# Kernel optimization log

Measured on AMD Instinct MI355X. Metric: run time of the kernel, lower is better.

Reference implementation:

```python
import jax, jax.numpy as jnp
import numpy as np

DIM = 512; H = 8; TEMP_LEN = 16; TARGET_LEN = 22
NT = TEMP_LEN ** 2          # 256 temp tokens
NS = TARGET_LEN ** 2        # 484 target tokens
N = NT + NS                 # 740
HD = DIM // H
SCALE = HD ** -0.5
EPS = 1e-5
B = 16


def _bias_index(L):
    coords = np.stack(np.meshgrid(np.arange(L), np.arange(L), indexing='ij')).reshape(2, -1)
    rel = (coords[:, :, None] - coords[:, None, :]).transpose(1, 2, 0)  # [L^2, L^2, 2]
    rel[..., 0] += L - 1
    rel[..., 1] += L - 1
    rel[..., 0] *= 2 * L - 1
    return jnp.asarray(rel.sum(-1))  # [L^2, L^2] indices into (2L-1)^2 table

TEMP_IDX = _bias_index(TEMP_LEN)
TARGET_IDX = _bias_index(TARGET_LEN)


def setup_inputs() -> dict:
    key = jax.random.key(0)
    ctr = iter(range(100))
    def nrm(shape, s=1.0):
        return jax.random.normal(jax.random.fold_in(key, next(ctr)), shape, jnp.float32) * s
    def uni(shape):
        return jax.random.uniform(jax.random.fold_in(key, next(ctr)), shape, jnp.float32, 0.5, 1.5)
    d = {'x': nrm((B, N, DIM))}
    for nm in ('q', 'k', 'v'):
        d[f'conv_{nm}_w'] = nrm((DIM, 1, 3, 3), 0.2)   # depthwise 3x3, groups=DIM
        d[f'bn_{nm}_g'] = 1.0 + nrm((DIM,), 0.1)
        d[f'bn_{nm}_b'] = nrm((DIM,), 0.1)
        d[f'bn_{nm}_m'] = nrm((DIM,), 0.1)
        d[f'bn_{nm}_v'] = uni((DIM,))
    for nm in ('q', 'k', 'v', 'p'):
        d[f'w{nm}'] = nrm((DIM, DIM), DIM ** -0.5)
        d[f'b{nm}'] = nrm((DIM,), 0.01)
    d['rpb_target'] = nrm(((2 * TARGET_LEN - 1) ** 2, H), 0.0002)
    d['rpb_temp'] = nrm(((2 * TEMP_LEN - 1) ** 2, 1), 0.0002)
    d['tt_bias'] = nrm((H, 1, NT), 0.0002)       # temp_target_bias_table
    d['tg_tm_bias'] = nrm((H, NS, 1), 0.0002)    # target_temp_bias_table
    return d


def _dwconv_bn(z, w, g, b, m, v):
    # z: [B, C, Hh, Ww]; depthwise conv + BatchNorm2d (inference stats)
    y = jax.lax.conv_general_dilated(z, w, (1, 1), ((1, 1), (1, 1)),
                                     dimension_numbers=('NCHW', 'OIHW', 'NCHW'),
                                     feature_group_count=DIM)
    inv = (g * jax.lax.rsqrt(v + EPS))[None, :, None, None]
    return (y - m[None, :, None, None]) * inv + b[None, :, None, None]


def reference(x, conv_q_w, bn_q_g, bn_q_b, bn_q_m, bn_q_v,
              conv_k_w, bn_k_g, bn_k_b, bn_k_m, bn_k_v,
              conv_v_w, bn_v_g, bn_v_b, bn_v_m, bn_v_v,
              wq, bq, wk, bk, wv, bv, wp, bp,
              rpb_target, rpb_temp, tt_bias, tg_tm_bias):
    Bb = x.shape[0]
    to_img = lambda t, L: t.transpose(0, 2, 1).reshape(Bb, DIM, L, L)
    to_seq = lambda t: t.reshape(Bb, DIM, -1).transpose(0, 2, 1)
    ti = to_img(x[:, :NT], TEMP_LEN)
    tg = to_img(x[:, NT:], TARGET_LEN)

    def conv_branch(w, g, b, m, v):
        return jnp.concatenate([to_seq(_dwconv_bn(ti, w, g, b, m, v)),
                                to_seq(_dwconv_bn(tg, w, g, b, m, v))], axis=1)

    q = conv_branch(conv_q_w, bn_q_g, bn_q_b, bn_q_m, bn_q_v) @ wq + bq
    k = conv_branch(conv_k_w, bn_k_g, bn_k_b, bn_k_m, bn_k_v) @ wk + bk
    v = conv_branch(conv_v_w, bn_v_g, bn_v_b, bn_v_m, bn_v_v) @ wv + bv

    heads = lambda t: t.reshape(Bb, -1, H, HD).transpose(0, 2, 1, 3)
    qtm, ktm, vtm = heads(q[:, :NT]), heads(k[:, :NT]), heads(v[:, :NT])
    qta, kh, vh = heads(q[:, NT:]), heads(k), heads(v)

    # gathered relative-position bias tables
    target_bias = rpb_target[TARGET_IDX.reshape(-1)].reshape(NS, NS, H).transpose(2, 0, 1)  # [H,NS,NS]
    temp_bias = rpb_temp[TEMP_IDX.reshape(-1)].reshape(NT, NT, 1).transpose(2, 0, 1)        # [1,NT,NT]
    padding = tt_bias + tg_tm_bias                                                          # [H,NS,NT]
    rel = jnp.concatenate([padding, target_bias], axis=2)                                   # [H,NS,N]

    # target -> all attention
    attn = jax.nn.softmax(jnp.einsum('bhqd,bhkd->bhqk', qta, kh) * SCALE + rel, axis=-1)
    out_t = jnp.einsum('bhqk,bhkd->bhqd', attn, vh).transpose(0, 2, 1, 3).reshape(Bb, NS, DIM)

    # temp -> temp attention (bias broadcast over heads)
    attn2 = jax.nn.softmax(jnp.einsum('bhqd,bhkd->bhqk', qtm, ktm) * SCALE + temp_bias, axis=-1)
    out_m = jnp.einsum('bhqk,bhkd->bhqd', attn2, vtm).transpose(0, 2, 1, 3).reshape(Bb, NT, DIM)

    return jnp.concatenate([out_m, out_t], axis=1) @ wp + bp
```

## Files before the change

kernel.cpp:

```cpp
#include <hip/hip_runtime.h>
#include <hip/hip_bf16.h>

typedef unsigned short u16;
typedef unsigned int u32;
typedef __attribute__((ext_vector_type(8))) short short8;
typedef __attribute__((ext_vector_type(4))) float f32x4;

#define NTOK 740
#define NTMP 256
#define NTGT 484
#define DM   512
#define MH   8
#define MROWS 11840
#define KPAD 768
#define LOG2E 1.4426950408889634f

__device__ __forceinline__ float b2f(u16 u) {
    union { unsigned int i; float f; } x; x.i = ((unsigned int)u) << 16; return x.f;
}
__device__ __forceinline__ u16 f2b(float f) {
    union { float f; unsigned int i; } x; x.f = f;
    unsigned int r = x.i + 0x7FFFu + ((x.i >> 16) & 1u);
    return (u16)(r >> 16);
}
__device__ __forceinline__ u32 pk2(float a, float b) {
    union { __hip_bfloat162 h; u32 u; } p;
    p.h = __float22bfloat162_rn(float2{a, b});
    return p.u;
}
__device__ __forceinline__ float fexp2(float x) {
    return __builtin_amdgcn_exp2f(x);
}
struct alignas(8) us4 { u16 x, y, z, w; };

__device__ __forceinline__ void gload16(const void* g, void* l) {
    __builtin_amdgcn_global_load_lds(
        (const __attribute__((address_space(1))) void*)g,
        (__attribute__((address_space(3))) void*)l, 16, 0, 0);
}

__global__ __launch_bounds__(256) void transpose4(const float* __restrict__ w0,
                                                  const float* __restrict__ w1,
                                                  const float* __restrict__ w2,
                                                  const float* __restrict__ w3,
                                                  u16* __restrict__ wTbase) {
    __shared__ float t[32][33];
    const int z = blockIdx.z;
    const float* W = z == 0 ? w0 : z == 1 ? w1 : z == 2 ? w2 : w3;
    u16* WT = wTbase + (size_t)z * 262144;
    int bx = blockIdx.x, by = blockIdx.y;
    int tx = threadIdx.x;
    for (int i = threadIdx.y; i < 32; i += 8)
        t[i][tx] = W[(size_t)(by * 32 + i) * 512 + bx * 32 + tx];
    __syncthreads();
    for (int i = threadIdx.y; i < 32; i += 8)
        WT[(size_t)(bx * 32 + i) * 512 + by * 32 + tx] = f2b(t[tx][i]);
}

__global__ __launch_bounds__(512) void prep_conv3(
    const float* __restrict__ cw0, const float* __restrict__ g0, const float* __restrict__ bb0,
    const float* __restrict__ m0, const float* __restrict__ v0,
    const float* __restrict__ cw1, const float* __restrict__ g1, const float* __restrict__ bb1,
    const float* __restrict__ m1, const float* __restrict__ v1,
    const float* __restrict__ cw2, const float* __restrict__ g2, const float* __restrict__ bb2,
    const float* __restrict__ m2, const float* __restrict__ v2,
    float* __restrict__ cwfb, float* __restrict__ shb) {
    const int tap = blockIdx.x, br = blockIdx.y, c = threadIdx.x;
    const float* cw = br == 0 ? cw0 : br == 1 ? cw1 : cw2;
    const float* g  = br == 0 ? g0  : br == 1 ? g1  : g2;
    const float* bb = br == 0 ? bb0 : br == 1 ? bb1 : bb2;
    const float* m  = br == 0 ? m0  : br == 1 ? m1  : m2;
    const float* v  = br == 0 ? v0  : br == 1 ? v1  : v2;
    const float inv = g[c] * rsqrtf(v[c] + 1e-5f);
    cwfb[(br * 9 + tap) * DM + c] = cw[c * 9 + tap] * inv;
    if (tap == 0) shb[br * DM + c] = bb[c] - m[c] * inv;
}

__global__ __launch_bounds__(256) void conv_bn3(
    const float* __restrict__ x,
    const float* __restrict__ cwfb, const float* __restrict__ shb,
    u16* __restrict__ o0, u16* __restrict__ o1, u16* __restrict__ o2) {
    const int bn = blockIdx.x * 2 + (threadIdx.x >> 7);
    const int c = (threadIdx.x & 127) * 4;
    const int b = bn / NTOK, n = bn % NTOK;
    const bool tmp = n < NTMP;
    const int L = tmp ? 16 : 22, base = tmp ? 0 : NTMP, p = n - base;
    const int ph = p / L, pw = p % L;
    float4 xv[9];
#pragma unroll
    for (int tap = 0; tap < 9; ++tap) {
        const int dh = tap / 3 - 1, dw = tap % 3 - 1;
        const int h2 = ph + dh, w2 = pw + dw;
        const bool ok = (h2 >= 0 && h2 < L && w2 >= 0 && w2 < L);
        xv[tap] = ok ? *(const float4*)(x + (size_t)(b * NTOK + base + h2 * L + w2) * DM + c)
                     : float4{0.f, 0.f, 0.f, 0.f};
    }
    const size_t o = (size_t)bn * DM + c;
    u16* out[3] = {o0, o1, o2};
#pragma unroll
    for (int br = 0; br < 3; ++br) {
        float4 acc = *(const float4*)(shb + br * DM + c);
#pragma unroll
        for (int tap = 0; tap < 9; ++tap) {
            const float4 wv = *(const float4*)(cwfb + (br * 9 + tap) * DM + c);
            acc.x = fmaf(wv.x, xv[tap].x, acc.x);
            acc.y = fmaf(wv.y, xv[tap].y, acc.y);
            acc.z = fmaf(wv.z, xv[tap].z, acc.z);
            acc.w = fmaf(wv.w, xv[tap].w, acc.w);
        }
        us4 r;
        r.x = f2b(acc.x); r.y = f2b(acc.y); r.z = f2b(acc.z); r.w = f2b(acc.w);
        *(us4*)(out[br] + o) = r;
    }
}

#define GEMM_BODY(A, BT)                                                             \
    const int tid = threadIdx.x;                                                     \
    const int gm0 = blockIdx.x * 64;                                                 \
    const int gn0 = blockIdx.y * 128;                                                \
    const int lane = tid & 63, w = tid >> 6;                                         \
    const int lr = lane & 15, lg = lane >> 4;                                        \
    const int wm = (w >> 1) * 32, wn = (w & 1) * 64;                                 \
    const int srow4 = lane >> 2;                                                     \
    const int sc = (lane & 3) ^ (srow4 & 3);                                         \
    const u16* asrc  = A  + (size_t)(gm0 + w * 16 + srow4) * 512 + sc * 8;           \
    const u16* bsrc0 = BT + (size_t)(gn0 + w * 32 + srow4) * 512 + sc * 8;           \
    const u16* bsrc1 = BT + (size_t)(gn0 + w * 32 + 16 + srow4) * 512 + sc * 8;      \
    f32x4 acc[2][4] = {};                                                            \
    gload16(asrc, &As[0][w * 512]);                                                  \
    gload16(bsrc0, &Bs[0][w * 1024]);                                                \
    gload16(bsrc1, &Bs[0][w * 1024 + 512]);                                          \
    for (int kt = 0; kt < 16; ++kt) {                                                \
        const int cur = kt & 1;                                                      \
        if (kt < 15) {                                                               \
            gload16(asrc + (kt + 1) * 32, &As[cur ^ 1][w * 512]);                    \
            gload16(bsrc0 + (kt + 1) * 32, &Bs[cur ^ 1][w * 1024]);                  \
            gload16(bsrc1 + (kt + 1) * 32, &Bs[cur ^ 1][w * 1024 + 512]);            \
            asm volatile("s_waitcnt vmcnt(3)" ::: "memory");                         \
        } else {                                                                     \
            asm volatile("s_waitcnt vmcnt(0)" ::: "memory");                         \
        }                                                                            \
        __syncthreads();                                                             \
        short8 af[2], bfr[4];                                                        \
        _Pragma("unroll")                                                            \
        for (int i = 0; i < 2; ++i)                                                  \
            af[i] = *(const short8*)&As[cur][(wm + i * 16 + lr) * 32 + (lg ^ (lr & 3)) * 8]; \
        _Pragma("unroll")                                                            \
        for (int j = 0; j < 4; ++j)                                                  \
            bfr[j] = *(const short8*)&Bs[cur][(wn + j * 16 + lr) * 32 + (lg ^ (lr & 3)) * 8]; \
        _Pragma("unroll")                                                            \
        for (int i = 0; i < 2; ++i)                                                  \
            _Pragma("unroll")                                                        \
            for (int j = 0; j < 4; ++j)                                              \
                acc[i][j] = __builtin_amdgcn_mfma_f32_16x16x32_bf16(af[i], bfr[j], acc[i][j], 0, 0, 0); \
        __syncthreads();                                                             \
    }

__global__ __launch_bounds__(256) void gemm_qkv(
    const u16* __restrict__ Aq, const u16* __restrict__ Ak, const u16* __restrict__ Av,
    const u16* __restrict__ wTb, const float* __restrict__ bq,
    const float* __restrict__ bk, const float* __restrict__ bv,
    u16* __restrict__ qout, u16* __restrict__ kout, u16* __restrict__ vbT, int zbase) {
    __shared__ u16 As[2][64 * 32];
    __shared__ u16 Bs[2][128 * 32];
    const int z = blockIdx.z + zbase;
    const u16* A = z == 0 ? Aq : z == 1 ? Ak : Av;
    const u16* BT = wTb + (size_t)z * 262144;
    const float* bias = z == 0 ? bq : z == 1 ? bk : bv;
    GEMM_BODY(A, BT)
    u16* lin = z == 0 ? qout : kout;
#pragma unroll
    for (int i = 0; i < 2; ++i)
#pragma unroll
        for (int j = 0; j < 4; ++j) {
            const int gc = gn0 + wn + j * 16 + lr;
            const float bvl = bias[gc];
#pragma unroll
            for (int r = 0; r < 4; ++r) {
                const int gr = gm0 + wm + i * 16 + lg * 4 + r;
                const float val = acc[i][j][r] + bvl;
                if (z == 2) {
                    const int b2 = gr / NTOK, k = gr - b2 * NTOK;
                    const int hh = gc >> 6, d = gc & 63;
                    vbT[((size_t)(b2 * MH + hh) * 64 + d) * KPAD + k] = f2b(val);
                } else {
                    lin[(size_t)gr * 512 + gc] = f2b(val);
                }
            }
        }
}

__global__ __launch_bounds__(256) void gemm_out(const u16* __restrict__ Ain,
                                                const u16* __restrict__ BTin,
                                                const float* __restrict__ bias,
                                                float* __restrict__ C) {
    __shared__ u16 As[2][64 * 32];
    __shared__ u16 Bs[2][128 * 32];
    GEMM_BODY(Ain, BTin)
#pragma unroll
    for (int i = 0; i < 2; ++i)
#pragma unroll
        for (int j = 0; j < 4; ++j) {
            const int gc = gn0 + wn + j * 16 + lr;
            const float bvl = bias[gc];
#pragma unroll
            for (int r = 0; r < 4; ++r) {
                const int gr = gm0 + wm + i * 16 + lg * 4 + r;
                C[(size_t)gr * 512 + gc] = acc[i][j][r] + bvl;
            }
        }
}

__global__ __launch_bounds__(256) void build_bias_t(const float* __restrict__ rpb_t,
                                                    const float* __restrict__ tt,
                                                    const float* __restrict__ tg,
                                                    u16* __restrict__ btab) {
    const int q = blockIdx.x, h = blockIdx.y;
    const int qh = q / 22, qw = q % 22;
    const float tgv = tg[h * NTGT + q];
    for (int k = threadIdx.x; k < KPAD; k += 256) {
        float val;
        if (k < NTMP) val = (tt[h * NTMP + k] + tgv) * LOG2E;
        else if (k < NTOK) {
            const int kj = k - NTMP, kh = kj / 22, kw = kj % 22;
            val = rpb_t[((qh - kh + 21) * 43 + (qw - kw + 21)) * MH + h] * LOG2E;
        } else val = -1e30f;
        btab[((size_t)(h * NTGT + q)) * KPAD + k] = f2b(val);
    }
}
__global__ __launch_bounds__(256) void build_bias_m(const float* __restrict__ rpb_m,
                                                    u16* __restrict__ mtab) {
    const int q = blockIdx.x, k = threadIdx.x;
    const int qh = q >> 4, qw = q & 15, kh = k >> 4, kw = k & 15;
    mtab[q * 256 + k] = f2b(rpb_m[(qh - kh + 15) * 31 + (qw - kw + 15)] * LOG2E);
}

__global__ __launch_bounds__(256) void attn_all(const u16* __restrict__ qb,
                                                const u16* __restrict__ kb,
                                                const u16* __restrict__ vbT,
                                                const u16* __restrict__ btab,
                                                const u16* __restrict__ mtab,
                                                u16* __restrict__ attb) {
    __shared__ u16 Ks[2][32][64];
    __shared__ u16 VTs[2][64][32];
    __shared__ u16 Pb[4][16][32];

    const int bx = blockIdx.x, h = blockIdx.y, b = blockIdx.z;
    const bool tgt = bx < 8;
    const int q0 = (tgt ? bx : bx - 8) * 64;
    const int NKr = tgt ? NTOK : NTMP;
    const int NCH = tgt ? 24 : 8;
    const int QTOT = tgt ? NTGT : NTMP;
    const int QOFF = tgt ? NTMP : 0;
    const int tid = threadIdx.x;
    const int w = tid >> 6, lane = tid & 63;
    const int lq = lane & 15, lg = lane >> 4;
    const int fq = (lq & 3) ^ ((lq >> 2) & 3);
    const size_t brow = (size_t)b * NTOK;
    const float SCL = 0.125f * LOG2E;

    int qmine = q0 + w * 16 + lq;
    if (qmine > QTOT - 1) qmine = QTOT - 1;
    const u16* trow = tgt ? (btab + ((size_t)(h * NTGT + qmine)) * KPAD)
                          : (mtab + qmine * 256);

    short8 qf[2];
#pragma unroll
    for (int dc = 0; dc < 2; ++dc)
        qf[dc] = *(const short8*)(qb + (brow + QOFF + qmine) * DM + h * 64 + dc * 32 + lg * 8);

    const int krow = tid >> 3, ksc = tid & 7;
    const int vrow = tid >> 2, vsc = tid & 3;
    const int fv = (vrow & 3) ^ ((vrow >> 2) & 3);
    const u16* kptr = kb + brow * DM + h * 64 + ksc * 8;
    const u16* vptr = vbT + (size_t)(b * MH + h) * 64 * KPAD + (size_t)vrow * KPAD + vsc * 8;

    float mrun = -1e30f, lrun = 0.f;
    f32x4 oT[4] = {};

    {
        int4 kv = (krow < NKr) ? *(const int4*)(kptr + (size_t)krow * DM) : int4{0, 0, 0, 0};
        *(int4*)&Ks[0][krow][(ksc ^ (krow & 7)) * 8] = kv;
        int4 vv = *(const int4*)(vptr);
        *(int4*)&VTs[0][vrow][(vsc ^ fv) * 8] = vv;
    }
    us4 bc0 = *(const us4*)(trow + lg * 4);
    us4 bc1 = *(const us4*)(trow + 16 + lg * 4);
    __syncthreads();

    for (int kc = 0; kc < NCH; ++kc) {
        const int cur = kc & 1, nxt = cur ^ 1;
        const bool more = (kc + 1 < NCH);
        int4 nk = {0, 0, 0, 0}, nv = {0, 0, 0, 0};
        us4 bn0 = {0, 0, 0, 0}, bn1 = {0, 0, 0, 0};
        if (more) {
            const int key = (kc + 1) * 32 + krow;
            if (key < NKr) nk = *(const int4*)(kptr + (size_t)key * DM);
            nv = *(const int4*)(vptr + (kc + 1) * 32);
            bn0 = *(const us4*)(trow + (kc + 1) * 32 + lg * 4);
            bn1 = *(const us4*)(trow + (kc + 1) * 32 + 16 + lg * 4);
        }

        f32x4 s0 = {}, s1 = {};
        __builtin_amdgcn_s_setprio(1);
#pragma unroll
        for (int dc = 0; dc < 2; ++dc) {
            short8 a0 = *(const short8*)&Ks[cur][lq][((dc * 4 + lg) ^ (lq & 7)) * 8];
            short8 a1 = *(const short8*)&Ks[cur][16 + lq][((dc * 4 + lg) ^ (lq & 7)) * 8];
            s0 = __builtin_amdgcn_mfma_f32_16x16x32_bf16(a0, qf[dc], s0, 0, 0, 0);
            s1 = __builtin_amdgcn_mfma_f32_16x16x32_bf16(a1, qf[dc], s1, 0, 0, 0);
        }
        __builtin_amdgcn_s_setprio(0);
        float sv[8];
        sv[0] = fmaf(s0[0], SCL, b2f(bc0.x)); sv[1] = fmaf(s0[1], SCL, b2f(bc0.y));
        sv[2] = fmaf(s0[2], SCL, b2f(bc0.z)); sv[3] = fmaf(s0[3], SCL, b2f(bc0.w));
        sv[4] = fmaf(s1[0], SCL, b2f(bc1.x)); sv[5] = fmaf(s1[1], SCL, b2f(bc1.y));
        sv[6] = fmaf(s1[2], SCL, b2f(bc1.z)); sv[7] = fmaf(s1[3], SCL, b2f(bc1.w));

        float cm = sv[0];
#pragma unroll
        for (int i = 1; i < 8; ++i) cm = fmaxf(cm, sv[i]);
        cm = fmaxf(cm, __shfl_xor(cm, 16));
        cm = fmaxf(cm, __shfl_xor(cm, 32));
        if (!__all(cm <= mrun)) {
            const float mnew = fmaxf(mrun, cm);
            const float alpha = fexp2(mrun - mnew);
#pragma unroll
            for (int t = 0; t < 4; ++t)
#pragma unroll
                for (int r = 0; r < 4; ++r) oT[t][r] *= alpha;
            lrun *= alpha;
            mrun = mnew;
        }
        float pv[8]; float psum = 0.f;
#pragma unroll
        for (int i = 0; i < 8; ++i) { pv[i] = fexp2(sv[i] - mrun); psum += pv[i]; }

        const int c0 = (((lg >> 1) ^ fq) & 3) * 8 + (lg & 1) * 4;
        const int c1 = (((2 + (lg >> 1)) ^ fq) & 3) * 8 + (lg & 1) * 4;
        *(uint2*)&Pb[w][lq][c0] = uint2{pk2(pv[0], pv[1]), pk2(pv[2], pv[3])};
        *(uint2*)&Pb[w][lq][c1] = uint2{pk2(pv[4], pv[5]), pk2(pv[6], pv[7])};

        psum += __shfl_xor(psum, 16);
        psum += __shfl_xor(psum, 32);
        lrun += psum;

        asm volatile("s_waitcnt lgkmcnt(0)" ::: "memory");

        short8 pf = *(const short8*)&Pb[w][lq][((lg ^ fq) & 3) * 8];
        __builtin_amdgcn_s_setprio(1);
#pragma unroll
        for (int t = 0; t < 4; ++t) {
            short8 vf = *(const short8*)&VTs[cur][t * 16 + lq][((lg ^ fq) & 3) * 8];
            oT[t] = __builtin_amdgcn_mfma_f32_16x16x32_bf16(vf, pf, oT[t], 0, 0, 0);
        }
        __builtin_amdgcn_s_setprio(0);

        if (more) {
            *(int4*)&Ks[nxt][krow][(ksc ^ (krow & 7)) * 8] = nk;
            *(int4*)&VTs[nxt][vrow][(vsc ^ fv) * 8] = nv;
            bc0 = bn0; bc1 = bn1;
        }
        __syncthreads();
    }

    const float linv = 1.f / lrun;
    const int qrow = q0 + w * 16 + lq;
    if (qrow < QTOT) {
        u16* op = attb + (brow + QOFF + qrow) * DM + h * 64;
#pragma unroll
        for (int t = 0; t < 4; ++t)
            *(uint2*)(op + t * 16 + lg * 4) =
                uint2{pk2(oT[t][0] * linv, oT[t][1] * linv),
                      pk2(oT[t][2] * linv, oT[t][3] * linv)};
    }
}

extern "C" void kernel_launch(void* const* d_in, const int* in_sizes, int n_in,
                              void* d_out, int out_size, void* d_ws, size_t ws_size,
                              hipStream_t stream) {
    const float* x = (const float*)d_in[0];
    const float* convw[3] = {(const float*)d_in[1], (const float*)d_in[6], (const float*)d_in[11]};
    const float* bng[3]   = {(const float*)d_in[2], (const float*)d_in[7], (const float*)d_in[12]};
    const float* bnb[3]   = {(const float*)d_in[3], (const float*)d_in[8], (const float*)d_in[13]};
    const float* bnm[3]   = {(const float*)d_in[4], (const float*)d_in[9], (const float*)d_in[14]};
    const float* bnv[3]   = {(const float*)d_in[5], (const float*)d_in[10], (const float*)d_in[15]};
    const float* w[4]     = {(const float*)d_in[16], (const float*)d_in[18], (const float*)d_in[20], (const float*)d_in[22]};
    const float* bias[4]  = {(const float*)d_in[17], (const float*)d_in[19], (const float*)d_in[21], (const float*)d_in[23]};
    const float* rpb_t = (const float*)d_in[24];
    const float* rpb_m = (const float*)d_in[25];
    const float* tt    = (const float*)d_in[26];
    const float* tg    = (const float*)d_in[27];

    char* ws = (char*)d_ws;
    u16* wTb = (u16*)ws;
    const size_t SEQ = (size_t)MROWS * DM * 2;
    u16* cbq  = (u16*)(ws + 2097152);
    u16* cbk  = (u16*)(ws + 2097152 + SEQ);
    u16* cbv  = (u16*)(ws + 2097152 + 2 * SEQ);
    u16* kbuf = (u16*)(ws + 2097152 + 3 * SEQ);
    u16* vbT  = (u16*)(ws + 2097152 + 4 * SEQ);
    u16* btab = (u16*)(ws + 2097152 + 4 * SEQ + 12582912);
    u16* mtab = (u16*)(ws + 2097152 + 4 * SEQ + 12582912 + 5947392);
    float* cwf = (float*)(ws + 2097152 + 4 * SEQ + 12582912 + 5947392 + 131072);
    float* shf = cwf + 3 * 9 * DM;
    u16* qbuf = cbv;
    u16* attb = cbq;

    transpose4<<<dim3(16, 16, 4), dim3(32, 8), 0, stream>>>(w[0], w[1], w[2], w[3], wTb);
    prep_conv3<<<dim3(9, 3), 512, 0, stream>>>(
        convw[0], bng[0], bnb[0], bnm[0], bnv[0],
        convw[1], bng[1], bnb[1], bnm[1], bnv[1],
        convw[2], bng[2], bnb[2], bnm[2], bnv[2], cwf, shf);
    build_bias_t<<<dim3(NTGT, MH), 256, 0, stream>>>(rpb_t, tt, tg, btab);
    build_bias_m<<<256, 256, 0, stream>>>(rpb_m, mtab);

    conv_bn3<<<MROWS / 2, 256, 0, stream>>>(x, cwf, shf, cbq, cbk, cbv);

    gemm_qkv<<<dim3(185, 4, 1), 256, 0, stream>>>(cbq, cbk, cbv, wTb,
                                                  bias[0], bias[1], bias[2],
                                                  qbuf, kbuf, vbT, 2);
    gemm_qkv<<<dim3(185, 4, 2), 256, 0, stream>>>(cbq, cbk, cbv, wTb,
                                                  bias[0], bias[1], bias[2],
                                                  qbuf, kbuf, vbT, 0);

    attn_all<<<dim3(12, 8, 16), 256, 0, stream>>>(qbuf, kbuf, vbT, btab, mtab, attb);

    gemm_out<<<dim3(185, 4), 256, 0, stream>>>(attb, wTb + 3 * 262144, bias[3], (float*)d_out);
}
```

Measured before the change: 186.3 us.

## Load K/V tiles directly global-to-LDS and remap workgroup order across XCDs

K and V tiles are now moved into shared memory with direct global-to-LDS loads (gload16), replacing the register round-trip and the explicit LDS stores. The swizzle is moved onto the global source address, and out-of-range keys are clamped to the last valid row instead of being zero-filled. The workgroup index is also remapped so that consecutive blocks of the same batch and head land on the same XCD, which is meant to improve L2 reuse of K/V. This adds a full vmcnt wait before each barrier, and clamped keys read duplicate data rather than zeros, which relies on the bias or masking handling those columns.

```diff
diff --git a/kernel.cpp b/kernel.cpp
--- a/kernel.cpp
+++ b/kernel.cpp
@@ -245,7 +245,12 @@
     __shared__ u16 VTs[2][64][32];
     __shared__ u16 Pb[4][16][32];
 
-    const int bx = blockIdx.x, h = blockIdx.y, b = blockIdx.z;
+    int wg = blockIdx.x + 12 * (blockIdx.y + 8 * blockIdx.z);
+    wg = (wg & 7) * 192 + (wg >> 3);
+    const int bx = wg % 12;
+    const int hb = wg / 12;
+    const int h = hb & 7, b = hb >> 3;
+
     const bool tgt = bx < 8;
     const int q0 = (tgt ? bx : bx - 8) * 64;
     const int NKr = tgt ? NTOK : NTMP;
@@ -272,31 +277,33 @@
     const int krow = tid >> 3, ksc = tid & 7;
     const int vrow = tid >> 2, vsc = tid & 3;
     const int fv = (vrow & 3) ^ ((vrow >> 2) & 3);
-    const u16* kptr = kb + brow * DM + h * 64 + ksc * 8;
-    const u16* vptr = vbT + (size_t)(b * MH + h) * 64 * KPAD + (size_t)vrow * KPAD + vsc * 8;
+    const size_t vbase = (size_t)(b * MH + h) * 64 * KPAD;
+    const u16* kptr2 = kb + brow * DM + h * 64 + (ksc ^ (krow & 7)) * 8;
+    const u16* vptr2 = vbT + vbase + (size_t)vrow * KPAD + (vsc ^ fv) * 8;
+    const int NKm1 = NKr - 1;
 
     float mrun = -1e30f, lrun = 0.f;
     f32x4 oT[4] = {};
 
     {
-        int4 kv = (krow < NKr) ? *(const int4*)(kptr + (size_t)krow * DM) : int4{0, 0, 0, 0};
-        *(int4*)&Ks[0][krow][(ksc ^ (krow & 7)) * 8] = kv;
-        int4 vv = *(const int4*)(vptr);
-        *(int4*)&VTs[0][vrow][(vsc ^ fv) * 8] = vv;
+        const int keyc = krow < NKm1 ? krow : NKm1;
+        gload16(kptr2 + (size_t)keyc * DM, &Ks[0][w * 8][0]);
+        gload16(vptr2, &VTs[0][w * 16][0]);
     }
     us4 bc0 = *(const us4*)(trow + lg * 4);
     us4 bc1 = *(const us4*)(trow + 16 + lg * 4);
+    asm volatile("s_waitcnt vmcnt(0)" ::: "memory");
     __syncthreads();
 
     for (int kc = 0; kc < NCH; ++kc) {
         const int cur = kc & 1, nxt = cur ^ 1;
         const bool more = (kc + 1 < NCH);
-        int4 nk = {0, 0, 0, 0}, nv = {0, 0, 0, 0};
         us4 bn0 = {0, 0, 0, 0}, bn1 = {0, 0, 0, 0};
         if (more) {
             const int key = (kc + 1) * 32 + krow;
-            if (key < NKr) nk = *(const int4*)(kptr + (size_t)key * DM);
-            nv = *(const int4*)(vptr + (kc + 1) * 32);
+            const int keyc = key < NKm1 ? key : NKm1;
+            gload16(kptr2 + (size_t)keyc * DM, &Ks[nxt][w * 8][0]);
+            gload16(vptr2 + (kc + 1) * 32, &VTs[nxt][w * 16][0]);
             bn0 = *(const us4*)(trow + (kc + 1) * 32 + lg * 4);
             bn1 = *(const us4*)(trow + (kc + 1) * 32 + 16 + lg * 4);
         }
@@ -356,11 +363,8 @@
         }
         __builtin_amdgcn_s_setprio(0);
 
-        if (more) {
-            *(int4*)&Ks[nxt][krow][(ksc ^ (krow & 7)) * 8] = nk;
-            *(int4*)&VTs[nxt][vrow][(vsc ^ fv) * 8] = nv;
-            bc0 = bn0; bc1 = bn1;
-        }
+        bc0 = bn0; bc1 = bn1;
+        asm volatile("s_waitcnt vmcnt(0)" ::: "memory");
         __syncthreads();
     }
 
```

Result: no change. 184.6 us (-0.9%).
